# Kernel tuning notes

Measured on AMD Instinct MI355X. Metric: run time of the kernel, lower is better.

Reference implementation:

```python
import jax, jax.numpy as jnp
import numpy as np

BIG_DIST = 1.0e7      # replaces NaN entries of the distance matrix (torch: where(isnan, 1e7))
BIG_DIFF = 10000.0    # nan_to_num value for cyclic coordinate error
MATCH_SAMPLE_NUM = 128


def setup_inputs() -> dict:
    key = jax.random.key(0)
    k1, k2, k3, k4, k5, k6 = jax.random.split(key, 6)
    b, h, w, c = 8, 64, 64, 384
    hw = h * w
    K = MATCH_SAMPLE_NUM
    return {
        "feature1": jax.random.normal(k1, (b, h, w, c), dtype=jnp.float32),
        "feature2": jax.random.normal(k2, (b, h, w, c), dtype=jnp.float32),
        "mask1": jax.random.randint(k3, (b, h, w, 1), 0, 2).astype(jnp.int32),
        "mask2": jax.random.randint(k4, (b, h, w, 1), 0, 2).astype(jnp.int32),
        "choose_backup1": jax.random.randint(k5, (b, K), 0, hw).astype(jnp.int32),
        "choose_backup2": jax.random.randint(k6, (b, K), 0, hw).astype(jnp.int32),
    }


def _masked_cdist(feature1, feature2, m1, m2):
    """Euclidean cdist of L2-normalized features; pairs touching a masked-out
    token get BIG_DIST (equivalent to torch's NaN-fill -> isnan -> 1e7)."""
    b, h, w, c = feature1.shape
    hw = h * w
    f1 = feature1.reshape(b, hw, c)
    f2 = feature2.reshape(b, hw, c)
    f1 = f1 / jnp.linalg.norm(f1, axis=-1, keepdims=True)
    f2 = f2 / jnp.linalg.norm(f2, axis=-1, keepdims=True)
    f1 = jnp.where(m1[..., None], f1, 0.0)
    f2 = jnp.where(m2[..., None], f2, 0.0)
    sq1 = jnp.sum(f1 * f1, axis=-1)              # [b, hw]
    sq2 = jnp.sum(f2 * f2, axis=-1)              # [b, hw]
    dots = jnp.einsum("bic,bjc->bij", f1, f2)    # [b, hw, hw]
    d2 = sq1[:, :, None] + sq2[:, None, :] - 2.0 * dots
    d = jnp.sqrt(jnp.maximum(d2, 0.0))
    valid_pair = m1[:, :, None] & m2[:, None, :]
    return jnp.where(valid_pair, d, BIG_DIST)


def _cyclic_diff(match_fwd, match_bwd, m_src, m_dst, h, w):
    """Cyclic-consistency coordinate error for each source token."""
    b, hw = match_fwd.shape
    # cyclic index: src -> dst (match_fwd) -> back to src (match_bwd gathered)
    dst_valid = jnp.take_along_axis(m_dst, match_fwd, axis=1)           # [b, hw]
    cyc = jnp.take_along_axis(match_bwd, match_fwd, axis=1)             # [b, hw]
    cx = (cyc // w).astype(jnp.float32)
    cy = (cyc % w).astype(jnp.float32)
    idx = jnp.arange(hw)
    gx = (idx // w).astype(jnp.float32)[None, :]
    gy = (idx % w).astype(jnp.float32)[None, :]
    diff = jnp.sqrt((cx - gx) ** 2 + (cy - gy) ** 2)
    valid = m_src & dst_valid
    return jnp.where(valid, diff, BIG_DIFF)


def reference(feature1, feature2, mask1, mask2, choose_backup1, choose_backup2):
    b, h, w, c = feature1.shape
    hw = h * w
    K = MATCH_SAMPLE_NUM
    m1 = mask1.reshape(b, hw) > 0
    m2 = mask2.reshape(b, hw) > 0

    d = _masked_cdist(feature1, feature2, m1, m2)   # [b, hw, hw]
    match1 = jnp.argmin(d, axis=-1)                 # best j for each i, [b, hw]
    match2 = jnp.argmin(d, axis=-2)                 # best i for each j, [b, hw]

    coord_diff1 = _cyclic_diff(match1, match2, m1, m2, h, w)
    coord_diff2 = _cyclic_diff(match2, match1, m2, m1, h, w)

    choose1 = jax.lax.top_k(-coord_diff1, K)[1]
    choose1 = jnp.where((jnp.sum(m1, axis=-1) >= K)[:, None], choose1, choose_backup1)
    choose1_match = jnp.take_along_axis(match1, choose1, axis=1)

    choose2 = jax.lax.top_k(-coord_diff2, K)[1]
    choose2 = jnp.where((jnp.sum(m2, axis=-1) >= K)[:, None], choose2, choose_backup2)
    choose2_match = jnp.take_along_axis(match2, choose2, axis=1)

    out_match1 = jnp.stack([choose1, choose1_match], axis=-1)   # [b, K, 2]
    out_match2 = jnp.stack([choose2, choose2_match], axis=-1)   # [b, K, 2]
    return out_match1, out_match2
```

## Files before the change

### kernel.cpp

```cpp
#include <hip/hip_runtime.h>
#include <stdint.h>

#define HW 4096
#define CH 384
#define NB 8
#define K_SEL 128
#define BIG_DIST 1.0e7f
#define BIG_DIFF 10000.0f
#define PAGE 8192
#define NKB 12
#define NRB 32

typedef unsigned long long u64;
typedef _Float16 f16;
typedef _Float16 f16x8 __attribute__((ext_vector_type(8)));
typedef float f32x4 __attribute__((ext_vector_type(4)));

__device__ __forceinline__ u64 encode_di(float d, int idx) {
    return ((u64)__float_as_uint(d) << 32) | (unsigned)idx;
}

__device__ __forceinline__ void gl_lds16(const void* g, void* l) {
    __builtin_amdgcn_global_load_lds(
        (const __attribute__((address_space(1))) unsigned int*)g,
        (__attribute__((address_space(3))) unsigned int*)l, 16, 0, 0);
}

__device__ __forceinline__ int swz(int row, int bytecol) {
    return (row * 64 + bytecol) ^ ((row & 7) << 4);
}

__global__ __launch_bounds__(1024)
void compact_mask(const int* __restrict__ mask1, const int* __restrict__ mask2,
                  int* __restrict__ vidx1, int* __restrict__ vidx2,
                  int* __restrict__ cpos1, int* __restrict__ cpos2,
                  u64* __restrict__ slot1, u64* __restrict__ slot2,
                  int* __restrict__ cnts) {
    const int b = blockIdx.x, which = blockIdx.y;
    const int* m = (which ? mask2 : mask1) + (size_t)b * HW;
    int* vidx = (which ? vidx2 : vidx1) + (size_t)b * HW;
    int* cpos = (which ? cpos2 : cpos1) + (size_t)b * HW;
    u64* slot = (which ? slot2 : slot1) + (size_t)b * HW;
    const int tid = threadIdx.x;
    const int lane = tid & 63, wv = tid >> 6;

    const int base = tid * 4;
    int4 mm = *(const int4*)(m + base);
    int v0 = mm.x > 0, v1 = mm.y > 0, v2 = mm.z > 0, v3 = mm.w > 0;
    int sum = v0 + v1 + v2 + v3;

    int inc = sum;
#pragma unroll
    for (int off = 1; off < 64; off <<= 1) {
        int o = __shfl_up(inc, off, 64);
        if (lane >= off) inc += o;
    }
    __shared__ int wtot[16], wbase[16];
    if (lane == 63) wtot[wv] = inc;
    __syncthreads();
    if (tid == 0) {
        int acc = 0;
        for (int w = 0; w < 16; ++w) { wbase[w] = acc; acc += wtot[w]; }
        cnts[b * 2 + which] = acc;
    }
    __syncthreads();
    int pos = wbase[wv] + inc - sum;
    if (v0) { vidx[pos] = base;     cpos[base]     = pos; pos++; } else cpos[base]     = -1;
    if (v1) { vidx[pos] = base + 1; cpos[base + 1] = pos; pos++; } else cpos[base + 1] = -1;
    if (v2) { vidx[pos] = base + 2; cpos[base + 2] = pos; pos++; } else cpos[base + 2] = -1;
    if (v3) { vidx[pos] = base + 3; cpos[base + 3] = pos; pos++; } else cpos[base + 3] = -1;
    __syncthreads();
    const int cnt = wbase[15] + wtot[15];
    for (int t = cnt + tid; t < HW; t += 1024) vidx[t] = 0;
    for (int t = tid; t < HW; t += 1024) slot[t] = ~0ULL;
}

__global__ __launch_bounds__(256)
void prep_tiles(const float* __restrict__ f1, const float* __restrict__ f2,
                const int* __restrict__ vidx1, const int* __restrict__ vidx2,
                const int* __restrict__ cnts,
                float* __restrict__ sqc1, float* __restrict__ sqc2,
                char* __restrict__ tA, char* __restrict__ tB) {
    const int lin = blockIdx.x;
    const int rb = lin % NRB;
    const int b = lin / NRB;
    const int which = blockIdx.y;
    const int cnt = cnts[b * 2 + which];
    const int rowbase = rb * 128;
    if (rowbase >= cnt) return;

    const float* f = which ? f2 : f1;
    const int* vidx = (which ? vidx2 : vidx1) + (size_t)b * HW;
    float* sqc = which ? sqc2 : sqc1;
    char* pages = (which ? tB : tA) + (size_t)lin * NKB * 2 * PAGE;
    const size_t bb = (size_t)b * HW;

    __shared__ float lds_rinv[128];
    __shared__ int lds_orig[128];

    const int tid = threadIdx.x, lane = tid & 63, wv = tid >> 6;

    for (int i = 0; i < 32; ++i) {
        int rl = wv * 32 + i;
        int r = rowbase + rl;
        int valid = r < cnt;
        int orig = vidx[r];
        const float* p = f + (bb + orig) * CH;
        float x[6];
        float s = 0.f;
#pragma unroll
        for (int t = 0; t < 6; ++t) { x[t] = p[lane + 64 * t]; s += x[t] * x[t]; }
#pragma unroll
        for (int off = 32; off >= 1; off >>= 1) s += __shfl_xor(s, off, 64);
        float rinv = 1.0f / __fsqrt_rn(s);
        float s2 = 0.f;
#pragma unroll
        for (int t = 0; t < 6; ++t) { float y = x[t] * rinv; s2 += y * y; }
#pragma unroll
        for (int off = 32; off >= 1; off >>= 1) s2 += __shfl_xor(s2, off, 64);
        if (lane == 0) {
            lds_rinv[rl] = valid ? rinv : 0.f;
            lds_orig[rl] = orig;
            sqc[bb + r] = valid ? s2 : 0.f;
        }
    }
    __syncthreads();

    for (int kb = 0; kb < NKB; ++kb) {
        char* hipg = pages + (size_t)kb * 2 * PAGE;
        char* lopg = hipg + PAGE;
#pragma unroll
        for (int p4 = 0; p4 < 4; ++p4) {
            int q = p4 * 256 + tid;
            int r = q >> 3;
            int kq = q & 7;
            int grow = lds_orig[r];
            float rv = lds_rinv[r];
            float4 x = *(const float4*)(f + (bb + grow) * CH + kb * 32 + kq * 4);
            x.x *= rv; x.y *= rv; x.z *= rv; x.w *= rv;
            f16 h0 = (f16)x.x, h1 = (f16)x.y, h2 = (f16)x.z, h3 = (f16)x.w;
            f16 l0 = (f16)((x.x - (float)h0) * 2048.0f);
            f16 l1 = (f16)((x.y - (float)h1) * 2048.0f);
            f16 l2 = (f16)((x.z - (float)h2) * 2048.0f);
            f16 l3 = (f16)((x.w - (float)h3) * 2048.0f);
            int off = swz(r, kq * 8);
            union { f16 h[4]; uint2 u; } H = {{h0, h1, h2, h3}};
            union { f16 h[4]; uint2 u; } L = {{l0, l1, l2, l3}};
            *(uint2*)(hipg + off) = H.u;
            *(uint2*)(lopg + off) = L.u;
        }
    }
}

__global__ __launch_bounds__(256, 3)
void gemm_argmin(const char* __restrict__ tA, const char* __restrict__ tB,
                 const float* __restrict__ sqc1, const float* __restrict__ sqc2,
                 const int* __restrict__ vidx1, const int* __restrict__ vidx2,
                 const int* __restrict__ cnts,
                 u64* __restrict__ slot1, u64* __restrict__ slot2) {
    __shared__ __align__(16) char smem[4 * PAGE];
    __shared__ u64 rowSlot[128];
    __shared__ u64 colSlot[128];

    const int b = blockIdx.y;
    const int tid = threadIdx.x;

    const int cnt1 = cnts[b * 2], cnt2 = cnts[b * 2 + 1];
    const int nby = (cnt1 + 127) >> 7;
    const int nbx = (cnt2 + 127) >> 7;
    const int nact = nby * nbx;

    const int xcd = blockIdx.x & 7;
    const int s = blockIdx.x >> 3;
    const int q = nact >> 3, r8 = nact & 7;
    const int csz = q + (xcd < r8 ? 1 : 0);
    if (s >= csz) return;
    const int L = (xcd < r8 ? xcd * (q + 1) : r8 * (q + 1) + (xcd - r8) * q) + s;
    const int bx = L / nby;
    const int by = L - bx * nby;
    const int brow = by * 128, bcol = bx * 128;

    const char* Abase = tA + (size_t)(b * NRB + by) * NKB * 2 * PAGE;
    const char* Bbase = tB + (size_t)(b * NRB + bx) * NKB * 2 * PAGE;

    const int wv = tid >> 6, lane = tid & 63;
    const int wr = wv >> 1, wc = wv & 1;
    const int r0 = lane & 15, kc = lane >> 4;

    int aoff[4], boff[4];
#pragma unroll
    for (int m = 0; m < 4; ++m) {
        int ra = wr * 64 + m * 16 + r0;
        aoff[m] = swz(ra, kc * 16);
        int rb_ = wc * 64 + m * 16 + r0;
        boff[m] = swz(rb_, kc * 16);
    }

    f32x4 acc[4][4];
    f32x4 zero = {0.f, 0.f, 0.f, 0.f};
#pragma unroll
    for (int m = 0; m < 4; ++m)
#pragma unroll
        for (int n = 0; n < 4; ++n) acc[m][n] = zero;

    const int stg = wv * 1024;
    const int src_l = stg + lane * 16;
    const f16 K2048 = (f16)2048.0f;

    for (int kb = 0; kb < NKB; ++kb) {
        const char* gA = Abase + (size_t)kb * 2 * PAGE;
        const char* gB = Bbase + (size_t)kb * 2 * PAGE;
#pragma unroll
        for (int p = 0; p < 4; ++p) {
            gl_lds16(gA + p * 4096 + src_l, smem + p * 4096 + stg);
            gl_lds16(gB + p * 4096 + src_l, smem + 16384 + p * 4096 + stg);
        }
        asm volatile("s_waitcnt vmcnt(0)" ::: "memory");
        __syncthreads();

        f16x8 bh[4], bl[4];
#pragma unroll
        for (int n = 0; n < 4; ++n) {
            bh[n] = *(const f16x8*)(smem + 2 * PAGE + boff[n]);
            bl[n] = *(const f16x8*)(smem + 3 * PAGE + boff[n]);
        }
#pragma unroll
        for (int m = 0; m < 4; ++m) {
            f16x8 ah = *(const f16x8*)(smem + aoff[m]);
            f16x8 al = *(const f16x8*)(smem + PAGE + aoff[m]);
            f16x8 ah2 = ah * K2048;
#pragma unroll
            for (int n = 0; n < 4; ++n) {
                acc[m][n] = __builtin_amdgcn_mfma_f32_16x16x32_f16(ah2, bh[n], acc[m][n], 0, 0, 0);
                acc[m][n] = __builtin_amdgcn_mfma_f32_16x16x32_f16(ah, bl[n], acc[m][n], 0, 0, 0);
                acc[m][n] = __builtin_amdgcn_mfma_f32_16x16x32_f16(al, bh[n], acc[m][n], 0, 0, 0);
            }
        }
        __syncthreads();
    }

    if (tid < 128) { rowSlot[tid] = ~0ULL; colSlot[tid] = ~0ULL; }
    __syncthreads();

    const size_t bb = (size_t)b * HW;
    const int rfrag = kc * 4;
    float s1v[4][4];
    int o1v[4][4], val1[4][4];
#pragma unroll
    for (int m = 0; m < 4; ++m) {
        int rr = brow + wr * 64 + m * 16 + rfrag;
        float4 sv = *(const float4*)(sqc1 + bb + rr);
        int4 ov = *(const int4*)(vidx1 + bb + rr);
        s1v[m][0] = sv.x; s1v[m][1] = sv.y; s1v[m][2] = sv.z; s1v[m][3] = sv.w;
        o1v[m][0] = ov.x; o1v[m][1] = ov.y; o1v[m][2] = ov.z; o1v[m][3] = ov.w;
#pragma unroll
        for (int j = 0; j < 4; ++j) val1[m][j] = (rr + j) < cnt1;
    }
    float s2v[4];
    int o2v[4], val2[4];
#pragma unroll
    for (int n = 0; n < 4; ++n) {
        int cc = bcol + wc * 64 + n * 16 + r0;
        s2v[n] = sqc2[bb + cc];
        o2v[n] = vidx2[bb + cc];
        val2[n] = cc < cnt2;
    }

    u64 cbest[4] = {~0ULL, ~0ULL, ~0ULL, ~0ULL};
#pragma unroll
    for (int m = 0; m < 4; ++m) {
#pragma unroll
        for (int j = 0; j < 4; ++j) {
            u64 rbest = ~0ULL;
#pragma unroll
            for (int n = 0; n < 4; ++n) {
                float d;
                if (val1[m][j] && val2[n]) {
                    float dot = acc[m][n][j] * (1.0f / 2048.0f);
                    float t = __fmul_rn(2.0f, dot);
                    float d2 = __fsub_rn(__fadd_rn(s1v[m][j], s2v[n]), t);
                    d = __fsqrt_rn(fmaxf(d2, 0.0f));
                } else {
                    d = BIG_DIST;
                }
                u64 er = encode_di(d, o2v[n]);
                u64 ec = encode_di(d, o1v[m][j]);
                if (er < rbest) rbest = er;
                if (ec < cbest[n]) cbest[n] = ec;
            }
            atomicMin(&rowSlot[wr * 64 + m * 16 + rfrag + j], rbest);
        }
    }
#pragma unroll
    for (int n = 0; n < 4; ++n)
        atomicMin(&colSlot[wc * 64 + n * 16 + r0], cbest[n]);
    __syncthreads();

    if (tid < 128) atomicMin(&slot1[bb + brow + tid], rowSlot[tid]);
    else           atomicMin(&slot2[bb + bcol + tid - 128], colSlot[tid - 128]);
}

__global__ void scatter_matches(const u64* __restrict__ slot1,
                                const u64* __restrict__ slot2,
                                const int* __restrict__ cpos1,
                                const int* __restrict__ cpos2,
                                int* __restrict__ match1, int* __restrict__ match2) {
    int g = blockIdx.x * blockDim.x + threadIdx.x;
    if (g >= NB * HW) return;
    int b = g >> 12;
    size_t bb = (size_t)b * HW;
    int p1 = cpos1[g];
    int v1 = 0;
    if (p1 >= 0) {
        u64 sv = slot1[bb + p1];
        if (sv != ~0ULL) v1 = (int)(unsigned)(sv & 0xFFFFFFFFu);
    }
    match1[g] = v1;
    int p2 = cpos2[g];
    int v2 = 0;
    if (p2 >= 0) {
        u64 sv = slot2[bb + p2];
        if (sv != ~0ULL) v2 = (int)(unsigned)(sv & 0xFFFFFFFFu);
    }
    match2[g] = v2;
}

__global__ __launch_bounds__(1024)
void topk_output(const int* __restrict__ match1, const int* __restrict__ match2,
                 const int* __restrict__ mask1, const int* __restrict__ mask2,
                 const int* __restrict__ backup1, const int* __restrict__ backup2,
                 int* __restrict__ out) {
    __shared__ u64 keys[HW];
    __shared__ u64 sel[K_SEL];
    __shared__ int hist[256];
    __shared__ int cnt, selc, sbuck, srank;
    const int b = blockIdx.x;
    const int dir = blockIdx.y;
    const int* mF = dir ? match2 : match1;
    const int* mB = dir ? match1 : match2;
    const int* maskS = dir ? mask2 : mask1;
    const int* maskD = dir ? mask1 : mask2;
    const int* backup = dir ? backup2 : backup1;
    const int tid = threadIdx.x;
    const size_t base = (size_t)b * HW;

    if (tid == 0) { cnt = 0; selc = 0; }
    __syncthreads();
    int local = 0;
    for (int t = tid; t < HW; t += 1024) {
        int mf = mF[base + t];
        int dv = maskD[base + mf];
        int cyc = mB[base + mf];
        float gx = (float)(t >> 6), gy = (float)(t & 63);
        float dx = (float)(cyc >> 6) - gx;
        float dy = (float)(cyc & 63) - gy;
        float diff = __fsqrt_rn(dx * dx + dy * dy);
        int ms = maskS[base + t];
        float v = (ms > 0 && dv > 0) ? diff : BIG_DIFF;
        keys[t] = encode_di(v, t);
        local += (ms > 0) ? 1 : 0;
    }
    atomicAdd(&cnt, local);
    __syncthreads();

    u64 prefix = 0;
    int rank = 127;
    for (int shift = 56; shift >= 0; shift -= 8) {
        for (int h = tid; h < 256; h += 1024) hist[h] = 0;
        __syncthreads();
        for (int t = tid; t < HW; t += 1024) {
            u64 k = keys[t];
            bool match = (shift == 56) || ((k >> (shift + 8)) == prefix);
            if (match) atomicAdd(&hist[(int)((k >> shift) & 255)], 1);
        }
        __syncthreads();
        if (tid < 64) {
            int v0 = hist[tid * 4 + 0], v1 = hist[tid * 4 + 1];
            int v2 = hist[tid * 4 + 2], v3 = hist[tid * 4 + 3];
            int s4 = v0 + v1 + v2 + v3;
            int inc = s4;
#pragma unroll
            for (int off = 1; off < 64; off <<= 1) {
                int o = __shfl_up(inc, off, 64);
                if (tid >= off) inc += o;
            }
            int c0 = inc - s4;
            int c1 = c0 + v0, c2 = c1 + v1, c3 = c2 + v2, c4 = c3 + v3;
            if (rank >= c0 && rank < c1)      { sbuck = tid * 4 + 0; srank = rank - c0; }
            else if (rank >= c1 && rank < c2) { sbuck = tid * 4 + 1; srank = rank - c1; }
            else if (rank >= c2 && rank < c3) { sbuck = tid * 4 + 2; srank = rank - c2; }
            else if (rank >= c3 && rank < c4) { sbuck = tid * 4 + 3; srank = rank - c3; }
        }
        __syncthreads();
        prefix = (prefix << 8) | (unsigned)sbuck;
        rank = srank;
        __syncthreads();
    }
    const u64 pivot = prefix;

    for (int t = tid; t < HW; t += 1024) {
        u64 k = keys[t];
        if (k <= pivot) { int p = atomicAdd(&selc, 1); sel[p] = k; }
    }
    __syncthreads();

    for (unsigned kk = 2; kk <= K_SEL; kk <<= 1) {
        for (unsigned j = kk >> 1; j > 0; j >>= 1) {
            if (tid < K_SEL) {
                unsigned ixj = tid ^ j;
                if (ixj > tid) {
                    u64 a = sel[tid], c = sel[ixj];
                    bool up = ((tid & kk) == 0);
                    if ((a > c) == up) { sel[tid] = c; sel[ixj] = a; }
                }
            }
            __syncthreads();
        }
    }

    if (tid < K_SEL) {
        int c;
        if (cnt >= K_SEL) c = (int)(unsigned)(sel[tid] & 0xFFFFFFFFu);
        else c = backup[b * K_SEL + tid];
        int cm = mF[base + c];
        int* o = out + dir * (NB * K_SEL * 2);
        o[(b * K_SEL + tid) * 2 + 0] = c;
        o[(b * K_SEL + tid) * 2 + 1] = cm;
    }
}

extern "C" void kernel_launch(void* const* d_in, const int* in_sizes, int n_in,
                              void* d_out, int out_size, void* d_ws, size_t ws_size,
                              hipStream_t stream) {
    const float* f1 = (const float*)d_in[0];
    const float* f2 = (const float*)d_in[1];
    const int* mask1 = (const int*)d_in[2];
    const int* mask2 = (const int*)d_in[3];
    const int* backup1 = (const int*)d_in[4];
    const int* backup2 = (const int*)d_in[5];
    int* out = (int*)d_out;

    char* ws = (char*)d_ws;
    char* tA = ws;                    ws += (size_t)NB * NRB * NKB * 2 * PAGE;
    char* tB = ws;                    ws += (size_t)NB * NRB * NKB * 2 * PAGE;
    u64* slot1 = (u64*)ws;            ws += (size_t)NB * HW * 8;
    u64* slot2 = (u64*)ws;            ws += (size_t)NB * HW * 8;
    float* sqc1 = (float*)ws;         ws += (size_t)NB * HW * 4;
    float* sqc2 = (float*)ws;         ws += (size_t)NB * HW * 4;
    int* vidx1 = (int*)ws;            ws += (size_t)NB * HW * 4;
    int* vidx2 = (int*)ws;            ws += (size_t)NB * HW * 4;
    int* cpos1 = (int*)ws;            ws += (size_t)NB * HW * 4;
    int* cpos2 = (int*)ws;            ws += (size_t)NB * HW * 4;
    int* match1 = (int*)ws;           ws += (size_t)NB * HW * 4;
    int* match2 = (int*)ws;           ws += (size_t)NB * HW * 4;
    int* cnts = (int*)ws;             ws += 256;

    const int nrows = NB * HW;

    compact_mask<<<dim3(NB, 2), 1024, 0, stream>>>(mask1, mask2,
                                                   vidx1, vidx2, cpos1, cpos2,
                                                   slot1, slot2, cnts);
    prep_tiles<<<dim3(NB * NRB, 2), 256, 0, stream>>>(f1, f2, vidx1, vidx2,
                                                      cnts, sqc1, sqc2, tA, tB);
    gemm_argmin<<<dim3(1024, NB), 256, 0, stream>>>(tA, tB, sqc1, sqc2,
                                                    vidx1, vidx2, cnts,
                                                    slot1, slot2);
    scatter_matches<<<(nrows + 255) / 256, 256, 0, stream>>>(slot1, slot2,
                                                             cpos1, cpos2,
                                                             match1, match2);
    topk_output<<<dim3(NB, 2), 1024, 0, stream>>>(match1, match2, mask1, mask2,
                                                  backup1, backup2, out);
}
```

Before: 187.4 us.

## Fuse match scatter into top-k, shrink radix keys, widen prep_tiles blocks

Removes the scatter_matches kernel and the match arrays: topk_output now resolves matches directly from the slot and cpos buffers when it needs them. The top-k sort key is repacked as float bits shifted by 12 with a 12-bit index, which cuts the radix select from eight passes to six. prep_tiles moves to 1024 threads per block so each thread handles one row/quad per k-block instead of looping four times. This saves a launch and global round-trip, but adds dependent gathers inside the single-block-per-batch top-k kernel.

```diff
diff --git a/kernel.cpp b/kernel.cpp
--- a/kernel.cpp
+++ b/kernel.cpp
@@ -75,7 +75,7 @@
     for (int t = tid; t < HW; t += 1024) slot[t] = ~0ULL;
 }
 
-__global__ __launch_bounds__(256)
+__global__ __launch_bounds__(1024)
 void prep_tiles(const float* __restrict__ f1, const float* __restrict__ f2,
                 const int* __restrict__ vidx1, const int* __restrict__ vidx2,
                 const int* __restrict__ cnts,
@@ -100,8 +100,9 @@
 
     const int tid = threadIdx.x, lane = tid & 63, wv = tid >> 6;
 
-    for (int i = 0; i < 32; ++i) {
-        int rl = wv * 32 + i;
+#pragma unroll
+    for (int i = 0; i < 8; ++i) {
+        int rl = wv * 8 + i;
         int r = rowbase + rl;
         int valid = r < cnt;
         int orig = vidx[r];
@@ -126,29 +127,26 @@
     }
     __syncthreads();
 
+    const int r = tid >> 3;
+    const int kq = tid & 7;
+    const int grow = lds_orig[r];
+    const float rv = lds_rinv[r];
+    const float* rowp = f + (bb + grow) * CH;
+    const int off = swz(r, kq * 8);
     for (int kb = 0; kb < NKB; ++kb) {
         char* hipg = pages + (size_t)kb * 2 * PAGE;
         char* lopg = hipg + PAGE;
-#pragma unroll
-        for (int p4 = 0; p4 < 4; ++p4) {
-            int q = p4 * 256 + tid;
-            int r = q >> 3;
-            int kq = q & 7;
-            int grow = lds_orig[r];
-            float rv = lds_rinv[r];
-            float4 x = *(const float4*)(f + (bb + grow) * CH + kb * 32 + kq * 4);
-            x.x *= rv; x.y *= rv; x.z *= rv; x.w *= rv;
-            f16 h0 = (f16)x.x, h1 = (f16)x.y, h2 = (f16)x.z, h3 = (f16)x.w;
-            f16 l0 = (f16)((x.x - (float)h0) * 2048.0f);
-            f16 l1 = (f16)((x.y - (float)h1) * 2048.0f);
-            f16 l2 = (f16)((x.z - (float)h2) * 2048.0f);
-            f16 l3 = (f16)((x.w - (float)h3) * 2048.0f);
-            int off = swz(r, kq * 8);
-            union { f16 h[4]; uint2 u; } H = {{h0, h1, h2, h3}};
-            union { f16 h[4]; uint2 u; } L = {{l0, l1, l2, l3}};
-            *(uint2*)(hipg + off) = H.u;
-            *(uint2*)(lopg + off) = L.u;
-        }
+        float4 x = *(const float4*)(rowp + kb * 32 + kq * 4);
+        x.x *= rv; x.y *= rv; x.z *= rv; x.w *= rv;
+        f16 h0 = (f16)x.x, h1 = (f16)x.y, h2 = (f16)x.z, h3 = (f16)x.w;
+        f16 l0 = (f16)((x.x - (float)h0) * 2048.0f);
+        f16 l1 = (f16)((x.y - (float)h1) * 2048.0f);
+        f16 l2 = (f16)((x.z - (float)h2) * 2048.0f);
+        f16 l3 = (f16)((x.w - (float)h3) * 2048.0f);
+        union { f16 h[4]; uint2 u; } H = {{h0, h1, h2, h3}};
+        union { f16 h[4]; uint2 u; } L = {{l0, l1, l2, l3}};
+        *(uint2*)(hipg + off) = H.u;
+        *(uint2*)(lopg + off) = L.u;
     }
 }
 
@@ -300,33 +298,18 @@
     else           atomicMin(&slot2[bb + bcol + tid - 128], colSlot[tid - 128]);
 }
 
-__global__ void scatter_matches(const u64* __restrict__ slot1,
-                                const u64* __restrict__ slot2,
-                                const int* __restrict__ cpos1,
-                                const int* __restrict__ cpos2,
-                                int* __restrict__ match1, int* __restrict__ match2) {
-    int g = blockIdx.x * blockDim.x + threadIdx.x;
-    if (g >= NB * HW) return;
-    int b = g >> 12;
-    size_t bb = (size_t)b * HW;
-    int p1 = cpos1[g];
-    int v1 = 0;
-    if (p1 >= 0) {
-        u64 sv = slot1[bb + p1];
-        if (sv != ~0ULL) v1 = (int)(unsigned)(sv & 0xFFFFFFFFu);
-    }
-    match1[g] = v1;
-    int p2 = cpos2[g];
-    int v2 = 0;
-    if (p2 >= 0) {
-        u64 sv = slot2[bb + p2];
-        if (sv != ~0ULL) v2 = (int)(unsigned)(sv & 0xFFFFFFFFu);
-    }
-    match2[g] = v2;
+__device__ __forceinline__ int get_match(const u64* __restrict__ slot,
+                                         const int* __restrict__ cpos,
+                                         size_t bb, int t) {
+    int p = cpos[bb + t];
+    if (p < 0) return 0;
+    u64 sv = slot[bb + p];
+    return (sv != ~0ULL) ? (int)(unsigned)(sv & 0xFFFFFFFFu) : 0;
 }
 
 __global__ __launch_bounds__(1024)
-void topk_output(const int* __restrict__ match1, const int* __restrict__ match2,
+void topk_output(const u64* __restrict__ slot1, const u64* __restrict__ slot2,
+                 const int* __restrict__ cpos1, const int* __restrict__ cpos2,
                  const int* __restrict__ mask1, const int* __restrict__ mask2,
                  const int* __restrict__ backup1, const int* __restrict__ backup2,
                  int* __restrict__ out) {
@@ -336,28 +319,30 @@
     __shared__ int cnt, selc, sbuck, srank;
     const int b = blockIdx.x;
     const int dir = blockIdx.y;
-    const int* mF = dir ? match2 : match1;
-    const int* mB = dir ? match1 : match2;
+    const u64* slotF = dir ? slot2 : slot1;
+    const u64* slotB = dir ? slot1 : slot2;
+    const int* cposF = dir ? cpos2 : cpos1;
+    const int* cposB = dir ? cpos1 : cpos2;
     const int* maskS = dir ? mask2 : mask1;
     const int* maskD = dir ? mask1 : mask2;
     const int* backup = dir ? backup2 : backup1;
     const int tid = threadIdx.x;
-    const size_t base = (size_t)b * HW;
+    const size_t bb = (size_t)b * HW;
 
     if (tid == 0) { cnt = 0; selc = 0; }
     __syncthreads();
     int local = 0;
     for (int t = tid; t < HW; t += 1024) {
-        int mf = mF[base + t];
-        int dv = maskD[base + mf];
-        int cyc = mB[base + mf];
+        int mf = get_match(slotF, cposF, bb, t);
+        int dv = maskD[bb + mf];
+        int cyc = get_match(slotB, cposB, bb, mf);
         float gx = (float)(t >> 6), gy = (float)(t & 63);
         float dx = (float)(cyc >> 6) - gx;
         float dy = (float)(cyc & 63) - gy;
         float diff = __fsqrt_rn(dx * dx + dy * dy);
-        int ms = maskS[base + t];
+        int ms = maskS[bb + t];
         float v = (ms > 0 && dv > 0) ? diff : BIG_DIFF;
-        keys[t] = encode_di(v, t);
+        keys[t] = ((u64)__float_as_uint(v) << 12) | (unsigned)t;
         local += (ms > 0) ? 1 : 0;
     }
     atomicAdd(&cnt, local);
@@ -365,12 +350,12 @@
 
     u64 prefix = 0;
     int rank = 127;
-    for (int shift = 56; shift >= 0; shift -= 8) {
+    for (int shift = 40; shift >= 0; shift -= 8) {
         for (int h = tid; h < 256; h += 1024) hist[h] = 0;
         __syncthreads();
         for (int t = tid; t < HW; t += 1024) {
             u64 k = keys[t];
-            bool match = (shift == 56) || ((k >> (shift + 8)) == prefix);
+            bool match = (shift == 40) || ((k >> (shift + 8)) == prefix);
             if (match) atomicAdd(&hist[(int)((k >> shift) & 255)], 1);
         }
         __syncthreads();
@@ -420,9 +405,9 @@
 
     if (tid < K_SEL) {
         int c;
-        if (cnt >= K_SEL) c = (int)(unsigned)(sel[tid] & 0xFFFFFFFFu);
+        if (cnt >= K_SEL) c = (int)(sel[tid] & 0xFFF);
         else c = backup[b * K_SEL + tid];
-        int cm = mF[base + c];
+        int cm = get_match(slotF, cposF, bb, c);
         int* o = out + dir * (NB * K_SEL * 2);
         o[(b * K_SEL + tid) * 2 + 0] = c;
         o[(b * K_SEL + tid) * 2 + 1] = cm;
@@ -451,23 +436,17 @@
     int* vidx2 = (int*)ws;            ws += (size_t)NB * HW * 4;
     int* cpos1 = (int*)ws;            ws += (size_t)NB * HW * 4;
     int* cpos2 = (int*)ws;            ws += (size_t)NB * HW * 4;
-    int* match1 = (int*)ws;           ws += (size_t)NB * HW * 4;
-    int* match2 = (int*)ws;           ws += (size_t)NB * HW * 4;
     int* cnts = (int*)ws;             ws += 256;
-
-    const int nrows = NB * HW;
 
     compact_mask<<<dim3(NB, 2), 1024, 0, stream>>>(mask1, mask2,
                                                    vidx1, vidx2, cpos1, cpos2,
                                                    slot1, slot2, cnts);
-    prep_tiles<<<dim3(NB * NRB, 2), 256, 0, stream>>>(f1, f2, vidx1, vidx2,
-                                                      cnts, sqc1, sqc2, tA, tB);
+    prep_tiles<<<dim3(NB * NRB, 2), 1024, 0, stream>>>(f1, f2, vidx1, vidx2,
+                                                       cnts, sqc1, sqc2, tA, tB);
     gemm_argmin<<<dim3(1024, NB), 256, 0, stream>>>(tA, tB, sqc1, sqc2,
                                                     vidx1, vidx2, cnts,
                                                     slot1, slot2);
-    scatter_matches<<<(nrows + 255) / 256, 256, 0, stream>>>(slot1, slot2,
-                                                             cpos1, cpos2,
-                                                             match1, match2);
-    topk_output<<<dim3(NB, 2), 1024, 0, stream>>>(match1, match2, mask1, mask2,
-                                                  backup1, backup2, out);
-}
+    topk_output<<<dim3(NB, 2), 1024, 0, stream>>>(slot1, slot2, cpos1, cpos2,
+                                                  mask1, mask2, backup1, backup2,
+                                                  out);
+}
```

Result: faster. 164.8 us (-12.0%).
